# Performance work log

Measured on AMD Instinct MI355X. Metric: run time of the kernel, lower is better.

## Reference

```python
import jax, jax.numpy as jnp
import numpy as np
import math

B, S, HID = 2, 2048, 2048
NH, NKV, HD, RD = 16, 4, 128, 64  # heads, kv heads, head_dim, rotary dim
G = NH // NKV                      # GQA group size = 4
EPS = 1e-6
THETA = 10000.0


def setup_inputs() -> dict:
    key = jax.random.key(0)
    k0, k1, k2 = jax.random.split(key, 3)
    hidden_states = jax.random.normal(k0, (B, S, HID), dtype=jnp.float32)
    # real rotary embeddings for rope_dim=64
    inv_freq = 1.0 / (THETA ** (jnp.arange(0, RD, 2, dtype=jnp.float32) / RD))  # [32]
    freqs = jnp.arange(S, dtype=jnp.float32)[:, None] * inv_freq[None, :]       # [S,32]
    emb = jnp.concatenate([freqs, freqs], axis=-1)                              # [S,64]
    cos = jnp.broadcast_to(jnp.cos(emb)[None], (B, S, RD)).astype(jnp.float32)
    sin = jnp.broadcast_to(jnp.sin(emb)[None], (B, S, RD)).astype(jnp.float32)
    w_qkv = jax.random.normal(k1, ((NH + 2 * NKV) * HD, HID), dtype=jnp.float32) * 0.02
    q_ln_w = jnp.ones((HD,), dtype=jnp.float32)
    k_ln_w = jnp.ones((HD,), dtype=jnp.float32)
    w_dense = jax.random.normal(k2, (HID, NH * HD), dtype=jnp.float32) * 0.02
    return {"hidden_states": hidden_states, "cos": cos, "sin": sin,
            "w_qkv": w_qkv, "q_ln_w": q_ln_w, "k_ln_w": k_ln_w, "w_dense": w_dense}


def _rmsnorm(x, w):
    xf = x.astype(jnp.float32)
    var = jnp.mean(xf * xf, axis=-1, keepdims=True)
    return (w * (xf * jax.lax.rsqrt(var + EPS)).astype(x.dtype))


def _rotate_half(x):
    x1, x2 = x[..., : x.shape[-1] // 2], x[..., x.shape[-1] // 2:]
    return jnp.concatenate([-x2, x1], axis=-1)


def reference(hidden_states, cos, sin, w_qkv, q_ln_w, k_ln_w, w_dense):
    bsz, q_len, _ = hidden_states.shape
    # fused QKV projection
    qkv = jnp.einsum('bsh,oh->bso', hidden_states, w_qkv)
    qkv = qkv.reshape(bsz, q_len, NH + 2 * NKV, HD)
    q = qkv[:, :, :NH].transpose(0, 2, 1, 3)            # [B,NH,S,HD]
    k = qkv[:, :, NH:NH + NKV].transpose(0, 2, 1, 3)    # [B,NKV,S,HD]
    v = qkv[:, :, NH + NKV:].transpose(0, 2, 1, 3)      # [B,NKV,S,HD]
    # per-head RMSNorm on Q/K
    q = _rmsnorm(q, q_ln_w)
    k = _rmsnorm(k, k_ln_w)
    # partial RoPE on first RD dims
    c = cos[:, None, :, :]  # [B,1,S,RD]
    s = sin[:, None, :, :]
    q_rot = q[..., :RD] * c + _rotate_half(q[..., :RD]) * s
    k_rot = k[..., :RD] * c + _rotate_half(k[..., :RD]) * s
    q = jnp.concatenate([q_rot, q[..., RD:]], axis=-1)
    k = jnp.concatenate([k_rot, k[..., RD:]], axis=-1)
    # GQA: group Q heads over KV heads (equivalent to repeat_kv)
    qg = q.reshape(bsz, NKV, G, q_len, HD)
    scale = 1.0 / math.sqrt(HD)
    scores = jnp.einsum('bgrqd,bgkd->bgrqk', qg, k) * scale   # [B,NKV,G,S,S]
    probs = jax.nn.softmax(scores.astype(jnp.float32), axis=-1).astype(q.dtype)
    out = jnp.einsum('bgrqk,bgkd->bgrqd', probs, v)           # [B,NKV,G,S,HD]
    out = out.reshape(bsz, NH, q_len, HD).transpose(0, 2, 1, 3).reshape(bsz, q_len, NH * HD)
    return jnp.einsum('bsd,od->bso', out, w_dense)
```

## Files before the change

### kernel.cpp

```cpp
#include <hip/hip_runtime.h>
#include <cstdint>
#include <cstddef>

typedef unsigned short u16;
typedef __attribute__((ext_vector_type(8))) short bf16x8;
typedef __attribute__((ext_vector_type(8))) u16   u16x8;
typedef __attribute__((ext_vector_type(4))) short short4v;
typedef __attribute__((ext_vector_type(4))) float f32x4;
typedef __attribute__((ext_vector_type(16))) float f32x16;
typedef __attribute__((ext_vector_type(4))) unsigned int u32x4;

#define DEVI static __device__ __forceinline__

constexpr int B_   = 2;
constexpr int S_   = 2048;
constexpr int HID_ = 2048;
constexpr int NH_  = 16;
constexpr int NKV_ = 4;
constexpr int HD_  = 128;
constexpr int TOK  = B_ * S_;
constexpr int OQKV = (NH_ + 2*NKV_) * HD_;

DEVI u16 f2bf(float f) {
  uint32_t u = __builtin_bit_cast(uint32_t, f);
  return (u16)((u + 0x7fffu + ((u >> 16) & 1u)) >> 16);
}
DEVI float bf2f(u16 h) { return __builtin_bit_cast(float, (uint32_t)h << 16); }

DEVI void gll16(const void* g, void* l) {
  __builtin_amdgcn_global_load_lds(
      (const __attribute__((address_space(1))) uint32_t*)g,
      (__attribute__((address_space(3))) uint32_t*)l, 16, 0, 0);
}

__global__ __launch_bounds__(256) void cvt_kernel(const float* __restrict__ in,
                                                  u16* __restrict__ out, int n8) {
  int idx = blockIdx.x * 256 + threadIdx.x;
  int stride = gridDim.x * 256;
  for (int i = idx; i < n8; i += stride) {
    const float4* p = reinterpret_cast<const float4*>(in) + (size_t)i * 2;
    float4 a = p[0], b = p[1];
    u16x8 v;
    v[0] = f2bf(a.x); v[1] = f2bf(a.y); v[2] = f2bf(a.z); v[3] = f2bf(a.w);
    v[4] = f2bf(b.x); v[5] = f2bf(b.y); v[6] = f2bf(b.z); v[7] = f2bf(b.w);
    reinterpret_cast<u16x8*>(out)[i] = v;
  }
}

template <bool OUT_BF16>
__global__ __launch_bounds__(256) void gemm_bt_kernel(
    const u16* __restrict__ A, const u16* __restrict__ B, void* __restrict__ Cv,
    int M, int N, int K) {
  constexpr int BM = 128, BN = 128, BK = 32;
  __shared__ __align__(16) u16 As[2][BM * BK];
  __shared__ __align__(16) u16 Bs[2][BN * BK];
  const int tid  = threadIdx.x;
  const int lane = tid & 63;
  const int wid  = tid >> 6;
  const int bm = blockIdx.x * BM;
  const int bn = blockIdx.y * BN;
  const int wm = (wid >> 1) * 64;
  const int wn = (wid & 1) * 64;
  const int fr = lane & 15, fg = lane >> 4;

  const f32x4 fzero = {0.f, 0.f, 0.f, 0.f};
  f32x4 acc[4][4];
#pragma unroll
  for (int m = 0; m < 4; m++)
#pragma unroll
    for (int n = 0; n < 4; n++) acc[m][n] = fzero;

  auto stage = [&](int buf, int k0) {
#pragma unroll
    for (int i = 0; i < 2; i++) {
      int e = i * 256 + tid;
      gll16(A + (size_t)(bm + (e >> 2)) * K + (k0 + (e & 3) * 8), &As[buf][e * 8]);
    }
#pragma unroll
    for (int i = 0; i < 2; i++) {
      int e = i * 256 + tid;
      gll16(B + (size_t)(bn + (e >> 2)) * K + (k0 + (e & 3) * 8), &Bs[buf][e * 8]);
    }
  };

  stage(0, 0);
  __syncthreads();
  const int nt = K / BK;
  for (int t = 0; t < nt; ++t) {
    int cur = t & 1;
    if (t + 1 < nt) stage(cur ^ 1, (t + 1) * BK);
    bf16x8 af[4], bfv[4];
#pragma unroll
    for (int m = 0; m < 4; m++)
      af[m] = *reinterpret_cast<const bf16x8*>(&As[cur][(wm + m * 16 + fr) * BK + fg * 8]);
#pragma unroll
    for (int n = 0; n < 4; n++)
      bfv[n] = *reinterpret_cast<const bf16x8*>(&Bs[cur][(wn + n * 16 + fr) * BK + fg * 8]);
#pragma unroll
    for (int m = 0; m < 4; m++)
#pragma unroll
      for (int n = 0; n < 4; n++)
        acc[m][n] = __builtin_amdgcn_mfma_f32_16x16x32_bf16(af[m], bfv[n], acc[m][n], 0, 0, 0);
    __syncthreads();
  }

#pragma unroll
  for (int m = 0; m < 4; m++)
#pragma unroll
    for (int n = 0; n < 4; n++)
#pragma unroll
      for (int j = 0; j < 4; j++) {
        size_t row = bm + wm + m * 16 + fg * 4 + j;
        size_t col = bn + wn + n * 16 + fr;
        if constexpr (OUT_BF16)
          reinterpret_cast<u16*>(Cv)[row * N + col] = f2bf(acc[m][n][j]);
        else
          reinterpret_cast<float*>(Cv)[row * N + col] = acc[m][n][j];
      }
}

__global__ __launch_bounds__(256) void rmsrope_kernel(
    const u16* __restrict__ qkv, const float* __restrict__ cosb,
    const float* __restrict__ sinb, const float* __restrict__ qw,
    const float* __restrict__ kw, u16* __restrict__ Q, u16* __restrict__ K) {
  int gw   = blockIdx.x * 4 + (threadIdx.x >> 6);
  int lane = threadIdx.x & 63;
  int tok  = gw / 20;
  int slot = gw - tok * 20;
  if (tok >= TOK) return;
  int b = tok >> 11, s = tok & (S_ - 1);
  const u16* src = qkv + (size_t)tok * OQKV + slot * HD_;
  float x0 = bf2f(src[lane]);
  float x1 = bf2f(src[lane + 64]);
  float ss = x0 * x0 + x1 * x1;
#pragma unroll
  for (int m = 1; m < 64; m <<= 1) ss += __shfl_xor(ss, m, 64);
  float r = rsqrtf(ss * (1.0f / 128.0f) + 1e-6f);
  const float* w = (slot < 16) ? qw : kw;
  x0 *= r * w[lane];
  x1 *= r * w[lane + 64];
  float c  = cosb[(size_t)tok * 64 + lane];
  float sn = sinb[(size_t)tok * 64 + lane];
  float partner = __shfl_xor(x0, 32, 64);
  float rot = (lane < 32) ? -partner : partner;
  x0 = x0 * c + rot * sn;
  u16* dst;
  if (slot < 16) dst = Q + (((size_t)b * NH_ + slot) * S_ + s) * HD_;
  else           dst = K + (((size_t)b * NKV_ + (slot - 16)) * S_ + s) * HD_;
  dst[lane]      = f2bf(x0);
  dst[lane + 64] = f2bf(x1);
}

__global__ __launch_bounds__(512, 2) void attn_kernel(
    const u16* __restrict__ Q, const u16* __restrict__ K,
    const u16* __restrict__ QKVb, u16* __restrict__ O) {
  __shared__ __align__(16) u16 Ks[2][64 * 128];
  __shared__ __align__(16) u16 Vt[2][128 * 64];
  __shared__ float rs_lds[8][32];
  const int tid  = threadIdx.x;
  const int lane = tid & 63, wid = tid >> 6;
  const int q32 = lane & 31, hi = lane >> 5;
  const int qt = blockIdx.x, bh = blockIdx.y;
  const int b = bh >> 4, h = bh & 15, kvh = h >> 2;

  const u16* Qrow  = Q + ((size_t)(b * NH_ + h) * S_ + qt * 256 + wid * 32 + q32) * HD_;
  const u16* Kbase = K + (size_t)(b * NKV_ + kvh) * S_ * HD_;
  const u16* Vbase = QKVb + (size_t)b * S_ * OQKV + (size_t)(NH_ + NKV_) * HD_ + (size_t)kvh * HD_;

  bf16x8 qf[8];
#pragma unroll
  for (int m = 0; m < 8; m++)
    qf[m] = *reinterpret_cast<const bf16x8*>(Qrow + m * 16 + hi * 8);

  f32x16 acc[4];
#pragma unroll
  for (int n = 0; n < 4; n++)
#pragma unroll
    for (int r = 0; r < 16; r++) acc[n][r] = 0.f;

  float rs = 0.f;
  const float scale = 0.08838834764831845f;

  auto stageK = [&](int buf, int kt) {
#pragma unroll
    for (int i = 0; i < 2; i++) {
      int e = i * 512 + tid;
      int krow = e >> 4, ci = e & 15;
      int cs = ci ^ (krow & 15);
      gll16(Kbase + ((size_t)kt * 64 + krow) * HD_ + cs * 8, &Ks[buf][e * 8]);
    }
  };
  u16x8 vreg[4];
  auto loadV = [&](int kt) {
    if (tid < 256) {
      int kvb = tid >> 4, db = tid & 15;
#pragma unroll
      for (int i = 0; i < 4; i++)
        vreg[i] = *reinterpret_cast<const u16x8*>(
            Vbase + ((size_t)kt * 64 + kvb * 4 + i) * OQKV + db * 8);
    }
  };
  auto writeV = [&](int buf) {
    if (tid < 256) {
      int kvb = tid >> 4, db = tid & 15;
#pragma unroll
      for (int j = 0; j < 8; j++) {
        int d = db * 8 + j;
        int sw = (d ^ (d >> 3)) & 7;
        int off = d * 128 + ((((kvb >> 1) ^ sw)) << 4) + ((kvb & 1) << 3);
        short4v wv = {(short)vreg[0][j], (short)vreg[1][j],
                      (short)vreg[2][j], (short)vreg[3][j]};
        *reinterpret_cast<short4v*>(reinterpret_cast<char*>(Vt[buf]) + off) = wv;
      }
    }
  };

  stageK(0, 0);
  loadV(0);
  writeV(0);
  __syncthreads();

  const int NT = S_ / 64;
  for (int kt = 0; kt < NT; ++kt) {
    const int cur = kt & 1;
    if (kt + 1 < NT) { stageK(cur ^ 1, kt + 1); loadV(kt + 1); }

    const u16* kbp = &Ks[cur][(size_t)q32 * 128];
    const int swz = lane & 15;
    unsigned int pa[4][4];
#pragma unroll
    for (int kb = 0; kb < 2; kb++) {
      f32x16 s;
#pragma unroll
      for (int r = 0; r < 16; r++) s[r] = 0.f;
      __builtin_amdgcn_s_setprio(1);
#pragma unroll
      for (int m = 0; m < 8; m++) {
        bf16x8 kf = *reinterpret_cast<const bf16x8*>(
            kbp + kb * 32 * 128 + ((((m * 2 + hi) ^ swz)) << 3));
        s = __builtin_amdgcn_mfma_f32_32x32x16_bf16(kf, qf[m], s, 0, 0, 0);
      }
      __builtin_amdgcn_s_setprio(0);
      float p[16];
#pragma unroll
      for (int r = 0; r < 16; r++) {
        p[r] = __expf(s[r] * scale);
        rs += p[r];
      }
      unsigned int w[8], x[8];
#pragma unroll
      for (int m2 = 0; m2 < 8; m2++)
        w[m2] = (unsigned int)f2bf(p[2 * m2]) | ((unsigned int)f2bf(p[2 * m2 + 1]) << 16);
#pragma unroll
      for (int m2 = 0; m2 < 8; m2++) x[m2] = __shfl_xor(w[m2], 32, 64);
#pragma unroll
      for (int tp = 0; tp < 2; tp++) {
        pa[kb * 2 + tp][0] = hi ? x[4 * tp + 2] : w[4 * tp + 0];
        pa[kb * 2 + tp][1] = hi ? x[4 * tp + 3] : w[4 * tp + 1];
        pa[kb * 2 + tp][2] = hi ? w[4 * tp + 2] : x[4 * tp + 0];
        pa[kb * 2 + tp][3] = hi ? w[4 * tp + 3] : x[4 * tp + 1];
      }
    }

#pragma unroll
    for (int t = 0; t < 4; t++) {
      union { u32x4 u; bf16x8 h; } pf;
      pf.u = (u32x4){pa[t][0], pa[t][1], pa[t][2], pa[t][3]};
      __builtin_amdgcn_s_setprio(1);
#pragma unroll
      for (int n = 0; n < 4; n++) {
        int d = n * 32 + q32;
        int sw = (d ^ (d >> 3)) & 7;
        bf16x8 vf = *reinterpret_cast<const bf16x8*>(
            reinterpret_cast<const char*>(Vt[cur]) + d * 128 + (((t * 2 + hi) ^ sw) << 4));
        acc[n] = __builtin_amdgcn_mfma_f32_32x32x16_bf16(pf.h, vf, acc[n], 0, 0, 0);
      }
      __builtin_amdgcn_s_setprio(0);
    }

    if (kt + 1 < NT) writeV(cur ^ 1);
    __syncthreads();
  }

  float rtot = rs + __shfl_xor(rs, 32, 64);
  if (lane < 32) rs_lds[wid][q32] = rtot;
  __syncthreads();
  float rinv[16];
#pragma unroll
  for (int r = 0; r < 16; r++)
    rinv[r] = 1.0f / rs_lds[wid][(r & 3) + 8 * (r >> 2) + 4 * hi];

  const int qrow0 = qt * 256 + wid * 32;
  u16* ob = O + ((size_t)b * S_ + qrow0) * HID_ + h * HD_ + q32;
#pragma unroll
  for (int n = 0; n < 4; n++)
#pragma unroll
    for (int r = 0; r < 16; r++) {
      int qr = (r & 3) + 8 * (r >> 2) + 4 * hi;
      ob[(size_t)qr * HID_ + n * 32] = f2bf(acc[n][r] * rinv[r]);
    }
}

extern "C" void kernel_launch(void* const* d_in, const int* in_sizes, int n_in,
                              void* d_out, int out_size, void* d_ws, size_t ws_size,
                              hipStream_t stream) {
  (void)in_sizes; (void)n_in; (void)out_size; (void)ws_size;
  const float* hs   = (const float*)d_in[0];
  const float* cosb = (const float*)d_in[1];
  const float* sinb = (const float*)d_in[2];
  const float* wqkv = (const float*)d_in[3];
  const float* qw   = (const float*)d_in[4];
  const float* kw   = (const float*)d_in[5];
  const float* wd   = (const float*)d_in[6];
  float* out = (float*)d_out;
  char* ws = (char*)d_ws;
  constexpr size_t MB = 1048576;
  u16* Xb    = (u16*)(ws + 0 * MB);
  u16* Wqkvb = (u16*)(ws + 16 * MB);
  u16* Wdb   = (u16*)(ws + 28 * MB);
  u16* QKVb  = (u16*)(ws + 36 * MB);
  u16* Qb    = (u16*)(ws + 60 * MB);
  u16* Kb    = (u16*)(ws + 76 * MB);
  u16* Ob    = (u16*)(ws + 80 * MB);

  cvt_kernel<<<2048, 256, 0, stream>>>(hs, Xb, TOK * HID_ / 8);
  cvt_kernel<<<2048, 256, 0, stream>>>(wqkv, Wqkvb, OQKV * HID_ / 8);
  cvt_kernel<<<1024, 256, 0, stream>>>(wd, Wdb, HID_ * HID_ / 8);

  gemm_bt_kernel<true><<<dim3(TOK / 128, OQKV / 128), 256, 0, stream>>>(
      Xb, Wqkvb, QKVb, TOK, OQKV, HID_);

  rmsrope_kernel<<<TOK * 20 / 4, 256, 0, stream>>>(QKVb, cosb, sinb, qw, kw, Qb, Kb);

  attn_kernel<<<dim3(S_ / 256, B_ * NH_), 512, 0, stream>>>(Qb, Kb, QKVb, Ob);

  gemm_bt_kernel<false><<<dim3(TOK / 128, HID_ / 128), 256, 0, stream>>>(
      Ob, Wdb, out, TOK, HID_, HID_);
}
```

Baseline: 227.5 us.

## Merge fp32-to-bf16 conversions into one launch and fold softmax scale into Q

Combines the three fp32-to-bf16 conversion launches into one kernel that loops over the three buffers, removing two launch overheads. The softmax scale times log2(e) is folded into Q during the RMSNorm/RoPE pass so attention can use exp2f directly, with no per-element multiply. The probability packing uses the hardware packed bf16 convert instruction instead of manual rounding. Q is now stored pre-scaled in bf16, which slightly changes rounding.

```diff
diff --git a/kernel.cpp b/kernel.cpp
--- a/kernel.cpp
+++ b/kernel.cpp
@@ -33,17 +33,25 @@
       (__attribute__((address_space(3))) uint32_t*)l, 16, 0, 0);
 }
 
-__global__ __launch_bounds__(256) void cvt_kernel(const float* __restrict__ in,
-                                                  u16* __restrict__ out, int n8) {
+__global__ __launch_bounds__(256) void cvt3_kernel(
+    const float* __restrict__ i0, u16* __restrict__ o0, int n0,
+    const float* __restrict__ i1, u16* __restrict__ o1, int n1,
+    const float* __restrict__ i2, u16* __restrict__ o2, int n2) {
   int idx = blockIdx.x * 256 + threadIdx.x;
   int stride = gridDim.x * 256;
-  for (int i = idx; i < n8; i += stride) {
-    const float4* p = reinterpret_cast<const float4*>(in) + (size_t)i * 2;
-    float4 a = p[0], b = p[1];
-    u16x8 v;
-    v[0] = f2bf(a.x); v[1] = f2bf(a.y); v[2] = f2bf(a.z); v[3] = f2bf(a.w);
-    v[4] = f2bf(b.x); v[5] = f2bf(b.y); v[6] = f2bf(b.z); v[7] = f2bf(b.w);
-    reinterpret_cast<u16x8*>(out)[i] = v;
+#pragma unroll 1
+  for (int pass = 0; pass < 3; ++pass) {
+    const float* in = pass == 0 ? i0 : pass == 1 ? i1 : i2;
+    u16* out       = pass == 0 ? o0 : pass == 1 ? o1 : o2;
+    int n8         = pass == 0 ? n0 : pass == 1 ? n1 : n2;
+    for (int i = idx; i < n8; i += stride) {
+      const float4* p = reinterpret_cast<const float4*>(in) + (size_t)i * 2;
+      float4 a = p[0], b = p[1];
+      u16x8 v;
+      v[0] = f2bf(a.x); v[1] = f2bf(a.y); v[2] = f2bf(a.z); v[3] = f2bf(a.w);
+      v[4] = f2bf(b.x); v[5] = f2bf(b.y); v[6] = f2bf(b.z); v[7] = f2bf(b.w);
+      reinterpret_cast<u16x8*>(out)[i] = v;
+    }
   }
 }
 
@@ -144,9 +152,14 @@
   float partner = __shfl_xor(x0, 32, 64);
   float rot = (lane < 32) ? -partner : partner;
   x0 = x0 * c + rot * sn;
+  const float QSC = 0.12751743f;
   u16* dst;
-  if (slot < 16) dst = Q + (((size_t)b * NH_ + slot) * S_ + s) * HD_;
-  else           dst = K + (((size_t)b * NKV_ + (slot - 16)) * S_ + s) * HD_;
+  if (slot < 16) {
+    x0 *= QSC; x1 *= QSC;
+    dst = Q + (((size_t)b * NH_ + slot) * S_ + s) * HD_;
+  } else {
+    dst = K + (((size_t)b * NKV_ + (slot - 16)) * S_ + s) * HD_;
+  }
   dst[lane]      = f2bf(x0);
   dst[lane + 64] = f2bf(x1);
 }
@@ -179,7 +192,6 @@
     for (int r = 0; r < 16; r++) acc[n][r] = 0.f;
 
   float rs = 0.f;
-  const float scale = 0.08838834764831845f;
 
   auto stageK = [&](int buf, int kt) {
 #pragma unroll
@@ -244,13 +256,16 @@
       float p[16];
 #pragma unroll
       for (int r = 0; r < 16; r++) {
-        p[r] = __expf(s[r] * scale);
+        p[r] = exp2f(s[r]);
         rs += p[r];
       }
       unsigned int w[8], x[8];
 #pragma unroll
-      for (int m2 = 0; m2 < 8; m2++)
-        w[m2] = (unsigned int)f2bf(p[2 * m2]) | ((unsigned int)f2bf(p[2 * m2 + 1]) << 16);
+      for (int m2 = 0; m2 < 8; m2++) {
+        unsigned int wv;
+        asm("v_cvt_pk_bf16_f32 %0, %1, %2" : "=v"(wv) : "v"(p[2 * m2]), "v"(p[2 * m2 + 1]));
+        w[m2] = wv;
+      }
 #pragma unroll
       for (int m2 = 0; m2 < 8; m2++) x[m2] = __shfl_xor(w[m2], 32, 64);
 #pragma unroll
@@ -323,9 +338,9 @@
   u16* Kb    = (u16*)(ws + 76 * MB);
   u16* Ob    = (u16*)(ws + 80 * MB);
 
-  cvt_kernel<<<2048, 256, 0, stream>>>(hs, Xb, TOK * HID_ / 8);
-  cvt_kernel<<<2048, 256, 0, stream>>>(wqkv, Wqkvb, OQKV * HID_ / 8);
-  cvt_kernel<<<1024, 256, 0, stream>>>(wd, Wdb, HID_ * HID_ / 8);
+  cvt3_kernel<<<2048, 256, 0, stream>>>(hs, Xb, TOK * HID_ / 8,
+                                        wqkv, Wqkvb, OQKV * HID_ / 8,
+                                        wd, Wdb, HID_ * HID_ / 8);
 
   gemm_bt_kernel<true><<<dim3(TOK / 128, OQKV / 128), 256, 0, stream>>>(
       Xb, Wqkvb, QKVb, TOK, OQKV, HID_);
```

New measurement: 227.5 us. About the same (+0.0%).
